# Kernel tuning notes

Hardware: AMD Instinct MI355X
Metric: run time of the kernel (lower is better)

Reference implementation:

```python
import jax, jax.numpy as jnp
import numpy as np
from jax import lax

EMB, HDIM, OBS_LEN = 64, 64, 8
BATCH, NSCENES, SCENE = 32768, 4096, 8
SEQ_LEN = 12


def setup_inputs() -> dict:
    key = jax.random.key(0)
    ks = jax.random.split(key, 16)
    obs_traj = jax.random.normal(ks[0], (OBS_LEN, BATCH, 2), jnp.float32)
    last_pos = jax.random.normal(ks[1], (BATCH, 2), jnp.float32)
    last_pos_rel = jax.random.normal(ks[2], (BATCH, 2), jnp.float32)
    starts = jnp.arange(NSCENES, dtype=jnp.int32) * SCENE
    seq_start_end = jnp.stack([starts, starts + SCENE], axis=1)  # (NSCENES, 2)
    # spatial_embedding: Linear(2, EMB)
    W_se = jax.random.normal(ks[3], (EMB, 2), jnp.float32) * 0.5
    b_se = jax.random.normal(ks[4], (EMB,), jnp.float32) * 0.1
    # weight-normed convs: w = g * v / ||v||_(in,k) per out-channel, bias init zero
    def conv_params(k, cout, cin, ksz):
        ka, kb = jax.random.split(k)
        std = np.sqrt(4.0 / (ksz * cin))
        v = jax.random.normal(ka, (cout, cin, ksz), jnp.float32) * std
        g = jax.random.uniform(kb, (cout,), jnp.float32, 0.5, 1.5)
        b = jnp.zeros((cout,), jnp.float32)
        return v, g, b
    v1, g1, b1 = conv_params(ks[5], HDIM, EMB, 3)
    v2, g2, b2 = conv_params(ks[6], HDIM // 2, HDIM, 3)
    v3, g3, b3 = conv_params(ks[7], HDIM // 2, HDIM // 2, 3)
    # hidden2pos: Linear(2*HDIM, 2)
    W_hp = jax.random.normal(ks[8], (2, 2 * HDIM), jnp.float32) * 0.05
    b_hp = jax.random.normal(ks[9], (2,), jnp.float32) * 0.05
    return {"obs_traj": obs_traj, "last_pos": last_pos, "last_pos_rel": last_pos_rel,
            "W_se": W_se, "b_se": b_se,
            "v1": v1, "g1": g1, "b1": b1,
            "v2": v2, "g2": g2, "b2": b2,
            "v3": v3, "g3": g3, "b3": b3,
            "W_hp": W_hp, "b_hp": b_hp,
            "seq_start_end": seq_start_end, "seq_len": SEQ_LEN}


def _wn_conv_relu(x, v, g, b):
    # weight-norm: w[o] = g[o] * v[o] / ||v[o]||  (norm over in-channels and kernel)
    norm = jnp.sqrt(jnp.sum(v * v, axis=(1, 2)))
    w = v * (g / norm)[:, None, None]
    y = lax.conv_general_dilated(x, w, (1,), 'VALID',
                                 dimension_numbers=('NCH', 'OIH', 'NCH'))
    return jax.nn.relu(y + b[None, :, None])


def reference(obs_traj, last_pos, last_pos_rel,
              W_se, b_se, v1, g1, b1, v2, g2, b2, v3, g3, b3, W_hp, b_hp,
              seq_start_end, seq_len):
    batch = last_pos.shape[0]
    nseg = seq_start_end.shape[0]
    h_dim = v1.shape[0]
    # scene id for each pedestrian (segments are contiguous [start,end) ranges)
    seg = jnp.searchsorted(seq_start_end[:, 0], jnp.arange(batch), side='right') - 1
    # obs_traj embedding -> (batch, EMB, OBS_LEN)
    emb = obs_traj @ W_se.T + b_se            # (T, B, EMB)
    obs_emb0 = jnp.transpose(emb, (1, 2, 0))  # (B, EMB, T)

    def step(carry, _):
        obs_emb, lp = carry
        s = _wn_conv_relu(obs_emb, v1, g1, b1)   # (B, H, T-2)
        s = _wn_conv_relu(s, v2, g2, b2)         # (B, H/2, T-4)
        s = _wn_conv_relu(s, v3, g3, b3)         # (B, H/2, T-6)
        s = s.reshape(batch, h_dim)              # (H/2)*(T-6) == H
        mx = jax.ops.segment_max(s, seg, num_segments=nseg)  # ragged per-scene max
        st = jnp.concatenate([s, mx[seg]], axis=1)           # (B, 2H)
        rel = st @ W_hp.T + b_hp                 # (B, 2)
        lp = rel + lp
        dec = rel @ W_se.T + b_se                # (B, EMB)
        obs_emb = jnp.concatenate([obs_emb[:, :, 1:], dec[:, :, None]], axis=2)
        return (obs_emb, lp), rel

    _, rels = lax.scan(step, (obs_emb0, last_pos), None, length=seq_len)
    return rels  # (seq_len, batch, 2)
```

## Files before the change

kernel.cpp:

```cpp
#include <hip/hip_runtime.h>

#define BATCH 32768
#define SEQLEN 12
#define PEDS 16
#define NBLK (BATCH/PEDS)

typedef short short8 __attribute__((ext_vector_type(8)));
typedef float f32x4 __attribute__((ext_vector_type(4)));

static __device__ __forceinline__ unsigned short f2bf(float x) {
    unsigned u = __float_as_uint(x);
    return (unsigned short)((u + 0x7FFFu + ((u >> 16) & 1u)) >> 16);
}
static __device__ __forceinline__ float bf2f(unsigned short h) {
    return __uint_as_float(((unsigned)h) << 16);
}
static __device__ __forceinline__ int mod6(int h) {
    h = (h >= 12) ? h - 12 : h;
    return (h >= 6) ? h - 6 : h;
}

__global__ __launch_bounds__(256, 3)
void enc_main(const float* __restrict__ obs,
              const float* __restrict__ Wse, const float* __restrict__ bse,
              const float* __restrict__ v1, const float* __restrict__ g1, const float* __restrict__ b1,
              const float* __restrict__ v2, const float* __restrict__ g2, const float* __restrict__ b2,
              const float* __restrict__ v3, const float* __restrict__ g3, const float* __restrict__ b3,
              const float* __restrict__ Whp, const float* __restrict__ bhp,
              float* __restrict__ out)
{
    __shared__ __align__(16) float pos[8][PEDS][2];
    __shared__ __align__(16) unsigned short s1h[6][PEDS][72], s1l[6][PEDS][72];
    __shared__ __align__(16) unsigned short s2h[4][PEDS][40], s2l[4][PEDS][40];
    __shared__ __align__(16) float sff[2][PEDS][68];
    __shared__ __align__(16) float mxs[2][2][68];

    float* wse_s = &sff[0][0][0];
    float* bse_s = wse_s + 128;
    float* sc_s  = wse_s + 192;
    float* a1c   = wse_s + 320;
    float* b1c   = wse_s + 512;
    float* c1c   = wse_s + 704;

    const int tid  = threadIdx.x;
    const int wv   = tid >> 6;
    const int lane = tid & 63;
    const int n    = lane & 15;
    const int kg   = lane >> 4;

    if (tid < 128) wse_s[tid] = Wse[tid];
    else if (tid < 192) bse_s[tid-128] = bse[tid-128];
    if (tid < 64) {
        const float* v = v1 + tid*192; float s = 0.f;
        for (int j = 0; j < 192; j++) s += v[j]*v[j];
        sc_s[tid] = g1[tid] / sqrtf(s);
    } else if (tid < 96) {
        const float* v = v2 + (tid-64)*192; float s = 0.f;
        for (int j = 0; j < 192; j++) s += v[j]*v[j];
        sc_s[tid] = g2[tid-64] / sqrtf(s);
    } else if (tid < 128) {
        const float* v = v3 + (tid-96)*96; float s = 0.f;
        for (int j = 0; j < 96; j++) s += v[j]*v[j];
        sc_s[tid] = g3[tid-96] / sqrtf(s);
    }
    __syncthreads();

    {
        int tau = tid >> 5, p = (tid >> 1) & 15, c = tid & 1;
        pos[tau][p][c] = obs[(tau*BATCH + blockIdx.x*PEDS + p)*2 + c];
    }
    if (tid < 192) {
        int oc = tid & 63, tap = tid >> 6;
        const float* vr = v1 + oc*192 + tap;
        float dA = 0.f, dB = 0.f, dC = 0.f;
        #pragma unroll 8
        for (int ic = 0; ic < 64; ++ic) {
            float w = vr[ic*3];
            dA = fmaf(w, wse_s[ic*2],   dA);
            dB = fmaf(w, wse_s[ic*2+1], dB);
            dC = fmaf(w, bse_s[ic],     dC);
        }
        a1c[tap*64+oc] = dA; b1c[tap*64+oc] = dB; c1c[tap*64+oc] = dC;
    }
    __syncthreads();

    const int c_p = tid >> 4, c_oc0 = (tid & 15) * 4;
    float cA[3][4], cB[3][4], K1[4];
    #pragma unroll
    for (int j = 0; j < 4; ++j) {
        int oc = c_oc0 + j; float s = sc_s[oc];
        float cs = 0.f;
        #pragma unroll
        for (int tap = 0; tap < 3; ++tap) {
            cA[tap][j] = s * a1c[tap*64+oc];
            cB[tap][j] = s * b1c[tap*64+oc];
            cs += c1c[tap*64+oc];
        }
        K1[j] = fmaf(s, cs, b1[oc]);
    }
    short8 wBh[6], wBl[6];
    float  bBr[4];
    if (wv < 2) {
        int oc = wv*16 + n; float s = sc_s[64 + oc];
        #pragma unroll
        for (int kb = 0; kb < 6; ++kb) {
            int tap = kb >> 1, ich = kb & 1;
            #pragma unroll
            for (int j = 0; j < 8; ++j) {
                int ic = ich*32 + kg*8 + j;
                float w = v2[(oc*64 + ic)*3 + tap] * s;
                unsigned short hb = f2bf(w);
                wBh[kb][j] = (short)hb;
                wBl[kb][j] = (short)f2bf(w - bf2f(hb));
            }
        }
        #pragma unroll
        for (int r = 0; r < 4; ++r) bBr[r] = b2[wv*16 + kg*4 + r];
    } else {
        int oc = (wv-2)*16 + n; float s = sc_s[96 + oc];
        #pragma unroll
        for (int kb = 0; kb < 3; ++kb) {
            #pragma unroll
            for (int j = 0; j < 8; ++j) {
                int ic = kg*8 + j;
                float w = v3[(oc*32 + ic)*3 + kb] * s;
                unsigned short hb = f2bf(w);
                wBh[kb][j] = (short)hb;
                wBl[kb][j] = (short)f2bf(w - bf2f(hb));
            }
        }
        #pragma unroll
        for (int r = 0; r < 4; ++r) bBr[r] = b3[(wv-2)*16 + kg*4 + r];
    }
    const int e_p = tid >> 4, e_d = (tid >> 3) & 1, e_sl = tid & 7;
    float wreg[16];
    #pragma unroll
    for (int j = 0; j < 16; ++j) wreg[j] = Whp[e_d*128 + e_sl*16 + j];
    const float bhps = bhp[e_d];

    for (int t = 0; t < 6; ++t) {
        float2 pa = *(const float2*)&pos[t  ][c_p][0];
        float2 pb = *(const float2*)&pos[t+1][c_p][0];
        float2 pc = *(const float2*)&pos[t+2][c_p][0];
        unsigned hw[2], lw[2];
        #pragma unroll
        for (int q = 0; q < 2; ++q) {
            float va, vb;
            {
                int j = q*2;
                va = K1[j];
                va = fmaf(cA[0][j], pa.x, va); va = fmaf(cB[0][j], pa.y, va);
                va = fmaf(cA[1][j], pb.x, va); va = fmaf(cB[1][j], pb.y, va);
                va = fmaf(cA[2][j], pc.x, va); va = fmaf(cB[2][j], pc.y, va);
                va = fmaxf(va, 0.f);
            }
            {
                int j = q*2+1;
                vb = K1[j];
                vb = fmaf(cA[0][j], pa.x, vb); vb = fmaf(cB[0][j], pa.y, vb);
                vb = fmaf(cA[1][j], pb.x, vb); vb = fmaf(cB[1][j], pb.y, vb);
                vb = fmaf(cA[2][j], pc.x, vb); vb = fmaf(cB[2][j], pc.y, vb);
                vb = fmaxf(vb, 0.f);
            }
            unsigned short ha = f2bf(va), hb = f2bf(vb);
            hw[q] = (unsigned)ha | ((unsigned)hb << 16);
            lw[q] = (unsigned)f2bf(va - bf2f(ha)) | ((unsigned)f2bf(vb - bf2f(hb)) << 16);
        }
        *(uint2*)&s1h[t][c_p][c_oc0] = make_uint2(hw[0], hw[1]);
        *(uint2*)&s1l[t][c_p][c_oc0] = make_uint2(lw[0], lw[1]);
    }
    __syncthreads();

    for (int st = 0; st < SEQLEN; ++st) {
        if (wv < 2) {
            for (int t = (st ? 3 : 0); t < 4; ++t) {
                f32x4 a1 = {0.f,0.f,0.f,0.f}, a2 = {0.f,0.f,0.f,0.f}, a3 = {0.f,0.f,0.f,0.f};
                #pragma unroll
                for (int kb = 0; kb < 6; ++kb) {
                    int slot = mod6(st + t + (kb >> 1));
                    int off  = (kb & 1)*32 + kg*8;
                    short8 bh = *(const short8*)&s1h[slot][n][off];
                    short8 bl = *(const short8*)&s1l[slot][n][off];
                    a1 = __builtin_amdgcn_mfma_f32_16x16x32_bf16(wBh[kb], bh, a1, 0, 0, 0);
                    a2 = __builtin_amdgcn_mfma_f32_16x16x32_bf16(wBh[kb], bl, a2, 0, 0, 0);
                    a3 = __builtin_amdgcn_mfma_f32_16x16x32_bf16(wBl[kb], bh, a3, 0, 0, 0);
                }
                int slot2 = (st + t) & 3, oc0 = wv*16 + kg*4;
                float v0 = fmaxf(a1[0]+a2[0]+a3[0]+bBr[0], 0.f);
                float v1_ = fmaxf(a1[1]+a2[1]+a3[1]+bBr[1], 0.f);
                float v2_ = fmaxf(a1[2]+a2[2]+a3[2]+bBr[2], 0.f);
                float v3_ = fmaxf(a1[3]+a2[3]+a3[3]+bBr[3], 0.f);
                unsigned short h0=f2bf(v0), h1=f2bf(v1_), h2=f2bf(v2_), h3=f2bf(v3_);
                *(uint2*)&s2h[slot2][n][oc0] = make_uint2(
                    (unsigned)h0 | ((unsigned)h1 << 16), (unsigned)h2 | ((unsigned)h3 << 16));
                *(uint2*)&s2l[slot2][n][oc0] = make_uint2(
                    (unsigned)f2bf(v0-bf2f(h0)) | ((unsigned)f2bf(v1_-bf2f(h1)) << 16),
                    (unsigned)f2bf(v2_-bf2f(h2)) | ((unsigned)f2bf(v3_-bf2f(h3)) << 16));
            }
        }
        __syncthreads();

        if (wv >= 2) {
            for (int t = (st ? 1 : 0); t < 2; ++t) {
                f32x4 a1 = {0.f,0.f,0.f,0.f}, a2 = {0.f,0.f,0.f,0.f}, a3 = {0.f,0.f,0.f,0.f};
                #pragma unroll
                for (int kb = 0; kb < 3; ++kb) {
                    int slot = (st + t + kb) & 3;
                    short8 bh = *(const short8*)&s2h[slot][n][kg*8];
                    short8 bl = *(const short8*)&s2l[slot][n][kg*8];
                    a1 = __builtin_amdgcn_mfma_f32_16x16x32_bf16(wBh[kb], bh, a1, 0, 0, 0);
                    a2 = __builtin_amdgcn_mfma_f32_16x16x32_bf16(wBh[kb], bl, a2, 0, 0, 0);
                    a3 = __builtin_amdgcn_mfma_f32_16x16x32_bf16(wBl[kb], bh, a3, 0, 0, 0);
                }
                int sl01 = (st + t) & 1, oc0 = (wv-2)*16 + kg*4;
                float m0 = fmaxf(a1[0]+a2[0]+a3[0]+bBr[0], 0.f);
                float m1 = fmaxf(a1[1]+a2[1]+a3[1]+bBr[1], 0.f);
                float m2 = fmaxf(a1[2]+a2[2]+a3[2]+bBr[2], 0.f);
                float m3 = fmaxf(a1[3]+a2[3]+a3[3]+bBr[3], 0.f);
                *(float4*)&sff[sl01][n][oc0] = make_float4(m0, m1, m2, m3);
                #pragma unroll
                for (int msk = 1; msk <= 4; msk <<= 1) {
                    m0 = fmaxf(m0, __shfl_xor(m0, msk));
                    m1 = fmaxf(m1, __shfl_xor(m1, msk));
                    m2 = fmaxf(m2, __shfl_xor(m2, msk));
                    m3 = fmaxf(m3, __shfl_xor(m3, msk));
                }
                if ((n & 7) == 0)
                    *(float4*)&mxs[sl01][n >> 3][oc0] = make_float4(m0, m1, m2, m3);
            }
        }
        __syncthreads();

        {
            int sE = st & 1, sO = (st + 1) & 1;
            float pv;
            if (e_sl < 4) {
                const float* A = &sff[sE][e_p][e_sl*8];
                const float* B = &sff[sO][e_p][e_sl*8];
                float4 a0 = *(const float4*)A, aq = *(const float4*)(A+4);
                float4 b0 = *(const float4*)B, bq = *(const float4*)(B+4);
                pv = wreg[0]*a0.x + wreg[1]*b0.x + wreg[2]*a0.y + wreg[3]*b0.y
                   + wreg[4]*a0.z + wreg[5]*b0.z + wreg[6]*a0.w + wreg[7]*b0.w
                   + wreg[8]*aq.x + wreg[9]*bq.x + wreg[10]*aq.y + wreg[11]*bq.y
                   + wreg[12]*aq.z + wreg[13]*bq.z + wreg[14]*aq.w + wreg[15]*bq.w;
            } else {
                int scn = e_p >> 3;
                const float* A = &mxs[sE][scn][(e_sl-4)*8];
                const float* B = &mxs[sO][scn][(e_sl-4)*8];
                float4 a0 = *(const float4*)A, aq = *(const float4*)(A+4);
                float4 b0 = *(const float4*)B, bq = *(const float4*)(B+4);
                pv = wreg[0]*a0.x + wreg[1]*b0.x + wreg[2]*a0.y + wreg[3]*b0.y
                   + wreg[4]*a0.z + wreg[5]*b0.z + wreg[6]*a0.w + wreg[7]*b0.w
                   + wreg[8]*aq.x + wreg[9]*bq.x + wreg[10]*aq.y + wreg[11]*bq.y
                   + wreg[12]*aq.z + wreg[13]*bq.z + wreg[14]*aq.w + wreg[15]*bq.w;
            }
            pv += __shfl_xor(pv, 1);
            pv += __shfl_xor(pv, 2);
            pv += __shfl_xor(pv, 4);
            float rm = pv + bhps;
            float ro = __shfl_xor(rm, 8);
            float r0 = e_d ? ro : rm;
            float r1 = e_d ? rm : ro;
            if (e_sl == 0)
                out[(st*BATCH + blockIdx.x*PEDS + e_p)*2 + e_d] = rm;
            if (st < SEQLEN-1) {
                float2 pa = *(const float2*)&pos[(st+6)&7][e_p][0];
                float2 pb = *(const float2*)&pos[(st+7)&7][e_p][0];
                int slot5 = mod6(st + 6);
                unsigned hw[2], lw[2];
                #pragma unroll
                for (int q = 0; q < 2; ++q) {
                    float va, vb;
                    {
                        int j = q*2;
                        va = K1[j];
                        va = fmaf(cA[0][j], pa.x, va); va = fmaf(cB[0][j], pa.y, va);
                        va = fmaf(cA[1][j], pb.x, va); va = fmaf(cB[1][j], pb.y, va);
                        va = fmaf(cA[2][j], r0,   va); va = fmaf(cB[2][j], r1,   va);
                        va = fmaxf(va, 0.f);
                    }
                    {
                        int j = q*2+1;
                        vb = K1[j];
                        vb = fmaf(cA[0][j], pa.x, vb); vb = fmaf(cB[0][j], pa.y, vb);
                        vb = fmaf(cA[1][j], pb.x, vb); vb = fmaf(cB[1][j], pb.y, vb);
                        vb = fmaf(cA[2][j], r0,   vb); vb = fmaf(cB[2][j], r1,   vb);
                        vb = fmaxf(vb, 0.f);
                    }
                    unsigned short ha = f2bf(va), hb = f2bf(vb);
                    hw[q] = (unsigned)ha | ((unsigned)hb << 16);
                    lw[q] = (unsigned)f2bf(va - bf2f(ha)) | ((unsigned)f2bf(vb - bf2f(hb)) << 16);
                }
                *(uint2*)&s1h[slot5][c_p][c_oc0] = make_uint2(hw[0], hw[1]);
                *(uint2*)&s1l[slot5][c_p][c_oc0] = make_uint2(lw[0], lw[1]);
                if (e_sl == 0)
                    pos[st & 7][e_p][e_d] = rm;
            }
        }
        __syncthreads();
    }
}

extern "C" void kernel_launch(void* const* d_in, const int* in_sizes, int n_in,
                              void* d_out, int out_size, void* d_ws, size_t ws_size,
                              hipStream_t stream)
{
    const float* obs = (const float*)d_in[0];
    const float* Wse = (const float*)d_in[3];
    const float* bse = (const float*)d_in[4];
    const float* v1  = (const float*)d_in[5];
    const float* g1  = (const float*)d_in[6];
    const float* b1  = (const float*)d_in[7];
    const float* v2  = (const float*)d_in[8];
    const float* g2  = (const float*)d_in[9];
    const float* b2  = (const float*)d_in[10];
    const float* v3  = (const float*)d_in[11];
    const float* g3  = (const float*)d_in[12];
    const float* b3  = (const float*)d_in[13];
    const float* Whp = (const float*)d_in[14];
    const float* bhp = (const float*)d_in[15];

    enc_main<<<NBLK, 256, 0, stream>>>(obs, Wse, bse, v1, g1, b1, v2, g2, b2,
                                       v3, g3, b3, Whp, bhp, (float*)d_out);
}
```

Baseline: 206.7 us.

## Restructure recurrence into two-wave pipeline with MFMA conv1 and register-resident state

The block shrinks from four waves to two. One wave does conv1 (now on MFMA with the weights split into hi and lo bf16 parts) and conv2. The other does conv3, the segment max and the hidden2pos projection, all from registers through shuffles, so the separate output phase and the shared sff/mxs buffers go away. Each step now has two barriers instead of three, ring buffers use &3 instead of mod6, and the bf16 split uses truncation instead of rounding. In exchange each wave carries more serial work and register pressure is higher, and with fewer threads per block there is less parallelism per block.

```diff
diff --git a/kernel.cpp b/kernel.cpp
--- a/kernel.cpp
+++ b/kernel.cpp
@@ -15,12 +15,15 @@
 static __device__ __forceinline__ float bf2f(unsigned short h) {
     return __uint_as_float(((unsigned)h) << 16);
 }
-static __device__ __forceinline__ int mod6(int h) {
-    h = (h >= 12) ? h - 12 : h;
-    return (h >= 6) ? h - 6 : h;
-}
-
-__global__ __launch_bounds__(256, 3)
+static __device__ __forceinline__ void tsplit2(float f0, float f1, unsigned &hw, unsigned &lw) {
+    unsigned u0 = __float_as_uint(f0), u1 = __float_as_uint(f1);
+    float r0 = f0 - __uint_as_float(u0 & 0xFFFF0000u);
+    float r1 = f1 - __uint_as_float(u1 & 0xFFFF0000u);
+    hw = (u0 >> 16) | (u1 & 0xFFFF0000u);
+    lw = (__float_as_uint(r0) >> 16) | (__float_as_uint(r1) & 0xFFFF0000u);
+}
+
+__global__ __launch_bounds__(128)
 void enc_main(const float* __restrict__ obs,
               const float* __restrict__ Wse, const float* __restrict__ bse,
               const float* __restrict__ v1, const float* __restrict__ g1, const float* __restrict__ b1,
@@ -29,27 +32,21 @@
               const float* __restrict__ Whp, const float* __restrict__ bhp,
               float* __restrict__ out)
 {
-    __shared__ __align__(16) float pos[8][PEDS][2];
-    __shared__ __align__(16) unsigned short s1h[6][PEDS][72], s1l[6][PEDS][72];
+    __shared__ __align__(16) unsigned short s1h[4][PEDS][72], s1l[4][PEDS][72];
     __shared__ __align__(16) unsigned short s2h[4][PEDS][40], s2l[4][PEDS][40];
-    __shared__ __align__(16) float sff[2][PEDS][68];
-    __shared__ __align__(16) float mxs[2][2][68];
-
-    float* wse_s = &sff[0][0][0];
-    float* bse_s = wse_s + 128;
-    float* sc_s  = wse_s + 192;
-    float* a1c   = wse_s + 320;
-    float* b1c   = wse_s + 512;
-    float* c1c   = wse_s + 704;
+    __shared__ float relL[PEDS][2];
+    __shared__ float wse_s[128], bse_s[64], sc_s[128];
+    __shared__ float a1c[192], b1c[192], c1c[192];
 
     const int tid  = threadIdx.x;
     const int wv   = tid >> 6;
     const int lane = tid & 63;
     const int n    = lane & 15;
     const int kg   = lane >> 4;
+    const int base = blockIdx.x * PEDS;
 
     if (tid < 128) wse_s[tid] = Wse[tid];
-    else if (tid < 192) bse_s[tid-128] = bse[tid-128];
+    if (tid < 64)  bse_s[tid] = bse[tid];
     if (tid < 64) {
         const float* v = v1 + tid*192; float s = 0.f;
         for (int j = 0; j < 192; j++) s += v[j]*v[j];
@@ -58,19 +55,15 @@
         const float* v = v2 + (tid-64)*192; float s = 0.f;
         for (int j = 0; j < 192; j++) s += v[j]*v[j];
         sc_s[tid] = g2[tid-64] / sqrtf(s);
-    } else if (tid < 128) {
+    } else {
         const float* v = v3 + (tid-96)*96; float s = 0.f;
         for (int j = 0; j < 96; j++) s += v[j]*v[j];
         sc_s[tid] = g3[tid-96] / sqrtf(s);
     }
     __syncthreads();
 
-    {
-        int tau = tid >> 5, p = (tid >> 1) & 15, c = tid & 1;
-        pos[tau][p][c] = obs[(tau*BATCH + blockIdx.x*PEDS + p)*2 + c];
-    }
-    if (tid < 192) {
-        int oc = tid & 63, tap = tid >> 6;
+    for (int idx = tid; idx < 192; idx += 128) {
+        int oc = idx & 63, tap = idx >> 6;
         const float* vr = v1 + oc*192 + tap;
         float dA = 0.f, dB = 0.f, dC = 0.f;
         #pragma unroll 8
@@ -80,222 +73,226 @@
             dB = fmaf(w, wse_s[ic*2+1], dB);
             dC = fmaf(w, bse_s[ic],     dC);
         }
-        a1c[tap*64+oc] = dA; b1c[tap*64+oc] = dB; c1c[tap*64+oc] = dC;
+        a1c[idx] = dA; b1c[idx] = dB; c1c[idx] = dC;
     }
     __syncthreads();
 
-    const int c_p = tid >> 4, c_oc0 = (tid & 15) * 4;
-    float cA[3][4], cB[3][4], K1[4];
-    #pragma unroll
-    for (int j = 0; j < 4; ++j) {
-        int oc = c_oc0 + j; float s = sc_s[oc];
-        float cs = 0.f;
-        #pragma unroll
-        for (int tap = 0; tap < 3; ++tap) {
-            cA[tap][j] = s * a1c[tap*64+oc];
-            cB[tap][j] = s * b1c[tap*64+oc];
-            cs += c1c[tap*64+oc];
-        }
-        K1[j] = fmaf(s, cs, b1[oc]);
+    short8 w2h[2][6], w2l[2][6];  float b2r[2][4];
+    short8 c1f[4];                f32x4 K1r[4];
+    unsigned pa_h=0, pa_l=0, pb_h=0, pb_l=0, pc_h=0, pc_l=0;
+    short8 w3h[2][3], w3l[2][3];  float b3r[2][4];
+    float Wsf[2][2][4][2], Wmx[2][2][4][2];
+    float bhp0=0.f, bhp1=0.f;
+    float prevv[2][4], prevmx[2][4];
+
+    auto conv1_col = [&](int slot, unsigned tAh, unsigned tAl, unsigned tBh, unsigned tBl,
+                         unsigned tCh, unsigned tCl) {
+        union { short8 v; unsigned u[4]; } B;
+        if (kg == 1)      { B.u[0]=tAl; B.u[1]=tBl; B.u[2]=tCl; }
+        else if (kg == 3) { B.u[0]=0u;  B.u[1]=0u;  B.u[2]=0u;  }
+        else              { B.u[0]=tAh; B.u[1]=tBh; B.u[2]=tCh; }
+        B.u[3] = 0u;
+        #pragma unroll
+        for (int T = 0; T < 4; ++T) {
+            f32x4 acc = __builtin_amdgcn_mfma_f32_16x16x32_bf16(c1f[T], B.v, K1r[T], 0, 0, 0);
+            float v0 = fmaxf(acc[0], 0.f), v1_ = fmaxf(acc[1], 0.f);
+            float v2_ = fmaxf(acc[2], 0.f), v3_ = fmaxf(acc[3], 0.f);
+            unsigned hw0, lw0, hw1, lw1;
+            tsplit2(v0, v1_, hw0, lw0);
+            tsplit2(v2_, v3_, hw1, lw1);
+            int o0 = T*16 + kg*4;
+            *(uint2*)&s1h[slot][n][o0] = make_uint2(hw0, hw1);
+            *(uint2*)&s1l[slot][n][o0] = make_uint2(lw0, lw1);
+        }
+    };
+
+    auto conv2_col = [&](int c) {
+        f32x4 A1[2] = {{0,0,0,0},{0,0,0,0}};
+        f32x4 A2[2] = {{0,0,0,0},{0,0,0,0}};
+        f32x4 A3[2] = {{0,0,0,0},{0,0,0,0}};
+        #pragma unroll
+        for (int kb = 0; kb < 6; ++kb) {
+            int slot = (c + (kb >> 1)) & 3;
+            int off  = (kb & 1)*32 + kg*8;
+            short8 bh = *(const short8*)&s1h[slot][n][off];
+            short8 bl = *(const short8*)&s1l[slot][n][off];
+            #pragma unroll
+            for (int T = 0; T < 2; ++T) {
+                A1[T] = __builtin_amdgcn_mfma_f32_16x16x32_bf16(w2h[T][kb], bh, A1[T], 0, 0, 0);
+                A2[T] = __builtin_amdgcn_mfma_f32_16x16x32_bf16(w2h[T][kb], bl, A2[T], 0, 0, 0);
+                A3[T] = __builtin_amdgcn_mfma_f32_16x16x32_bf16(w2l[T][kb], bh, A3[T], 0, 0, 0);
+            }
+        }
+        int s2s = c & 3;
+        #pragma unroll
+        for (int T = 0; T < 2; ++T) {
+            float v0 = fmaxf(A1[T][0]+A2[T][0]+A3[T][0]+b2r[T][0], 0.f);
+            float v1_ = fmaxf(A1[T][1]+A2[T][1]+A3[T][1]+b2r[T][1], 0.f);
+            float v2_ = fmaxf(A1[T][2]+A2[T][2]+A3[T][2]+b2r[T][2], 0.f);
+            float v3_ = fmaxf(A1[T][3]+A2[T][3]+A3[T][3]+b2r[T][3], 0.f);
+            unsigned hw0, lw0, hw1, lw1;
+            tsplit2(v0, v1_, hw0, lw0);
+            tsplit2(v2_, v3_, hw1, lw1);
+            int o0 = T*16 + kg*4;
+            *(uint2*)&s2h[s2s][n][o0] = make_uint2(hw0, hw1);
+            *(uint2*)&s2l[s2s][n][o0] = make_uint2(lw0, lw1);
+        }
+    };
+
+    auto conv3_col = [&](int c, float (&nv)[2][4], float (&nmx)[2][4]) {
+        f32x4 A1[2] = {{0,0,0,0},{0,0,0,0}};
+        f32x4 A2[2] = {{0,0,0,0},{0,0,0,0}};
+        f32x4 A3[2] = {{0,0,0,0},{0,0,0,0}};
+        #pragma unroll
+        for (int kb = 0; kb < 3; ++kb) {
+            int slot = (c + kb) & 3;
+            short8 bh = *(const short8*)&s2h[slot][n][kg*8];
+            short8 bl = *(const short8*)&s2l[slot][n][kg*8];
+            #pragma unroll
+            for (int T = 0; T < 2; ++T) {
+                A1[T] = __builtin_amdgcn_mfma_f32_16x16x32_bf16(w3h[T][kb], bh, A1[T], 0, 0, 0);
+                A2[T] = __builtin_amdgcn_mfma_f32_16x16x32_bf16(w3h[T][kb], bl, A2[T], 0, 0, 0);
+                A3[T] = __builtin_amdgcn_mfma_f32_16x16x32_bf16(w3l[T][kb], bh, A3[T], 0, 0, 0);
+            }
+        }
+        #pragma unroll
+        for (int T = 0; T < 2; ++T)
+            #pragma unroll
+            for (int r = 0; r < 4; ++r) {
+                float m = fmaxf(A1[T][r]+A2[T][r]+A3[T][r]+b3r[T][r], 0.f);
+                nv[T][r] = m;
+                m = fmaxf(m, __shfl_xor(m, 1));
+                m = fmaxf(m, __shfl_xor(m, 2));
+                m = fmaxf(m, __shfl_xor(m, 4));
+                nmx[T][r] = m;
+            }
+    };
+
+    if (wv == 0) {
+        #pragma unroll
+        for (int T = 0; T < 2; ++T) {
+            int oc = T*16 + n; float s = sc_s[64 + oc];
+            #pragma unroll
+            for (int kb = 0; kb < 6; ++kb) {
+                int tap = kb >> 1, ich = kb & 1;
+                #pragma unroll
+                for (int j = 0; j < 8; ++j) {
+                    int ic = ich*32 + kg*8 + j;
+                    float w = v2[(oc*64 + ic)*3 + tap] * s;
+                    unsigned short hb = f2bf(w);
+                    w2h[T][kb][j] = (short)hb;
+                    w2l[T][kb][j] = (short)f2bf(w - bf2f(hb));
+                }
+            }
+            #pragma unroll
+            for (int r = 0; r < 4; ++r) b2r[T][r] = b2[T*16 + kg*4 + r];
+        }
+        #pragma unroll
+        for (int T = 0; T < 4; ++T) {
+            int oc = T*16 + n; float s = sc_s[oc];
+            #pragma unroll
+            for (int j = 0; j < 8; ++j) {
+                float w = 0.f;
+                if (j < 6) {
+                    int tap = j >> 1;
+                    w = s * ((j & 1) ? b1c[tap*64 + oc] : a1c[tap*64 + oc]);
+                }
+                unsigned short hb = f2bf(w);
+                float wl = w - bf2f(hb);
+                c1f[T][j] = (kg <= 1) ? (short)hb : (kg == 2 ? (short)f2bf(wl) : (short)0);
+            }
+            #pragma unroll
+            for (int r = 0; r < 4; ++r) {
+                int o2 = T*16 + kg*4 + r;
+                K1r[T][r] = fmaf(sc_s[o2], c1c[o2] + c1c[64+o2] + c1c[128+o2], b1[o2]);
+            }
+        }
+        unsigned ph[8], pl[8];
+        #pragma unroll
+        for (int tau = 0; tau < 8; ++tau) {
+            float o0 = obs[(tau*BATCH + base + n)*2 + 0];
+            float o1 = obs[(tau*BATCH + base + n)*2 + 1];
+            tsplit2(o0, o1, ph[tau], pl[tau]);
+        }
+        conv1_col(0, ph[0],pl[0], ph[1],pl[1], ph[2],pl[2]);
+        conv1_col(1, ph[1],pl[1], ph[2],pl[2], ph[3],pl[3]);
+        conv1_col(2, ph[2],pl[2], ph[3],pl[3], ph[4],pl[4]);
+        conv1_col(3, ph[3],pl[3], ph[4],pl[4], ph[5],pl[5]);
+        conv2_col(0);
+        conv2_col(1);
+        conv1_col(0, ph[4],pl[4], ph[5],pl[5], ph[6],pl[6]);
+        conv1_col(1, ph[5],pl[5], ph[6],pl[6], ph[7],pl[7]);
+        conv2_col(2);
+        pa_h = ph[5]; pa_l = pl[5]; pb_h = ph[6]; pb_l = pl[6]; pc_h = ph[7]; pc_l = pl[7];
+    } else {
+        #pragma unroll
+        for (int T = 0; T < 2; ++T) {
+            int oc = T*16 + n; float s = sc_s[96 + oc];
+            #pragma unroll
+            for (int kb = 0; kb < 3; ++kb)
+                #pragma unroll
+                for (int j = 0; j < 8; ++j) {
+                    int ic = kg*8 + j;
+                    float w = v3[(oc*32 + ic)*3 + kb] * s;
+                    unsigned short hb = f2bf(w);
+                    w3h[T][kb][j] = (short)hb;
+                    w3l[T][kb][j] = (short)f2bf(w - bf2f(hb));
+                }
+            #pragma unroll
+            for (int r = 0; r < 4; ++r) b3r[T][r] = b3[T*16 + kg*4 + r];
+        }
+        #pragma unroll
+        for (int d2 = 0; d2 < 2; ++d2)
+            #pragma unroll
+            for (int T = 0; T < 2; ++T)
+                #pragma unroll
+                for (int r = 0; r < 4; ++r) {
+                    int oc = T*16 + kg*4 + r;
+                    #pragma unroll
+                    for (int t = 0; t < 2; ++t) {
+                        Wsf[d2][T][r][t] = Whp[d2*128 + oc*2 + t];
+                        Wmx[d2][T][r][t] = Whp[d2*128 + 64 + oc*2 + t];
+                    }
+                }
+        bhp0 = bhp[0]; bhp1 = bhp[1];
     }
-    short8 wBh[6], wBl[6];
-    float  bBr[4];
-    if (wv < 2) {
-        int oc = wv*16 + n; float s = sc_s[64 + oc];
-        #pragma unroll
-        for (int kb = 0; kb < 6; ++kb) {
-            int tap = kb >> 1, ich = kb & 1;
-            #pragma unroll
-            for (int j = 0; j < 8; ++j) {
-                int ic = ich*32 + kg*8 + j;
-                float w = v2[(oc*64 + ic)*3 + tap] * s;
-                unsigned short hb = f2bf(w);
-                wBh[kb][j] = (short)hb;
-                wBl[kb][j] = (short)f2bf(w - bf2f(hb));
-            }
-        }
-        #pragma unroll
-        for (int r = 0; r < 4; ++r) bBr[r] = b2[wv*16 + kg*4 + r];
-    } else {
-        int oc = (wv-2)*16 + n; float s = sc_s[96 + oc];
-        #pragma unroll
-        for (int kb = 0; kb < 3; ++kb) {
-            #pragma unroll
-            for (int j = 0; j < 8; ++j) {
-                int ic = kg*8 + j;
-                float w = v3[(oc*32 + ic)*3 + kb] * s;
-                unsigned short hb = f2bf(w);
-                wBh[kb][j] = (short)hb;
-                wBl[kb][j] = (short)f2bf(w - bf2f(hb));
-            }
-        }
-        #pragma unroll
-        for (int r = 0; r < 4; ++r) bBr[r] = b3[(wv-2)*16 + kg*4 + r];
-    }
-    const int e_p = tid >> 4, e_d = (tid >> 3) & 1, e_sl = tid & 7;
-    float wreg[16];
-    #pragma unroll
-    for (int j = 0; j < 16; ++j) wreg[j] = Whp[e_d*128 + e_sl*16 + j];
-    const float bhps = bhp[e_d];
-
-    for (int t = 0; t < 6; ++t) {
-        float2 pa = *(const float2*)&pos[t  ][c_p][0];
-        float2 pb = *(const float2*)&pos[t+1][c_p][0];
-        float2 pc = *(const float2*)&pos[t+2][c_p][0];
-        unsigned hw[2], lw[2];
-        #pragma unroll
-        for (int q = 0; q < 2; ++q) {
-            float va, vb;
-            {
-                int j = q*2;
-                va = K1[j];
-                va = fmaf(cA[0][j], pa.x, va); va = fmaf(cB[0][j], pa.y, va);
-                va = fmaf(cA[1][j], pb.x, va); va = fmaf(cB[1][j], pb.y, va);
-                va = fmaf(cA[2][j], pc.x, va); va = fmaf(cB[2][j], pc.y, va);
-                va = fmaxf(va, 0.f);
-            }
-            {
-                int j = q*2+1;
-                vb = K1[j];
-                vb = fmaf(cA[0][j], pa.x, vb); vb = fmaf(cB[0][j], pa.y, vb);
-                vb = fmaf(cA[1][j], pb.x, vb); vb = fmaf(cB[1][j], pb.y, vb);
-                vb = fmaf(cA[2][j], pc.x, vb); vb = fmaf(cB[2][j], pc.y, vb);
-                vb = fmaxf(vb, 0.f);
-            }
-            unsigned short ha = f2bf(va), hb = f2bf(vb);
-            hw[q] = (unsigned)ha | ((unsigned)hb << 16);
-            lw[q] = (unsigned)f2bf(va - bf2f(ha)) | ((unsigned)f2bf(vb - bf2f(hb)) << 16);
-        }
-        *(uint2*)&s1h[t][c_p][c_oc0] = make_uint2(hw[0], hw[1]);
-        *(uint2*)&s1l[t][c_p][c_oc0] = make_uint2(lw[0], lw[1]);
-    }
-    __syncthreads();
 
     for (int st = 0; st < SEQLEN; ++st) {
-        if (wv < 2) {
-            for (int t = (st ? 3 : 0); t < 4; ++t) {
-                f32x4 a1 = {0.f,0.f,0.f,0.f}, a2 = {0.f,0.f,0.f,0.f}, a3 = {0.f,0.f,0.f,0.f};
-                #pragma unroll
-                for (int kb = 0; kb < 6; ++kb) {
-                    int slot = mod6(st + t + (kb >> 1));
-                    int off  = (kb & 1)*32 + kg*8;
-                    short8 bh = *(const short8*)&s1h[slot][n][off];
-                    short8 bl = *(const short8*)&s1l[slot][n][off];
-                    a1 = __builtin_amdgcn_mfma_f32_16x16x32_bf16(wBh[kb], bh, a1, 0, 0, 0);
-                    a2 = __builtin_amdgcn_mfma_f32_16x16x32_bf16(wBh[kb], bl, a2, 0, 0, 0);
-                    a3 = __builtin_amdgcn_mfma_f32_16x16x32_bf16(wBl[kb], bh, a3, 0, 0, 0);
-                }
-                int slot2 = (st + t) & 3, oc0 = wv*16 + kg*4;
-                float v0 = fmaxf(a1[0]+a2[0]+a3[0]+bBr[0], 0.f);
-                float v1_ = fmaxf(a1[1]+a2[1]+a3[1]+bBr[1], 0.f);
-                float v2_ = fmaxf(a1[2]+a2[2]+a3[2]+bBr[2], 0.f);
-                float v3_ = fmaxf(a1[3]+a2[3]+a3[3]+bBr[3], 0.f);
-                unsigned short h0=f2bf(v0), h1=f2bf(v1_), h2=f2bf(v2_), h3=f2bf(v3_);
-                *(uint2*)&s2h[slot2][n][oc0] = make_uint2(
-                    (unsigned)h0 | ((unsigned)h1 << 16), (unsigned)h2 | ((unsigned)h3 << 16));
-                *(uint2*)&s2l[slot2][n][oc0] = make_uint2(
-                    (unsigned)f2bf(v0-bf2f(h0)) | ((unsigned)f2bf(v1_-bf2f(h1)) << 16),
-                    (unsigned)f2bf(v2_-bf2f(h2)) | ((unsigned)f2bf(v3_-bf2f(h3)) << 16));
-            }
+        if (wv == 0) {
+            if (st > 0) {
+                float r0 = relL[n][0], r1 = relL[n][1];
+                pa_h = pb_h; pa_l = pb_l; pb_h = pc_h; pb_l = pc_l;
+                tsplit2(r0, r1, pc_h, pc_l);
+                conv1_col((st + 5) & 3, pa_h, pa_l, pb_h, pb_l, pc_h, pc_l);
+            }
+            conv2_col(st + 3);
         }
         __syncthreads();
-
-        if (wv >= 2) {
-            for (int t = (st ? 1 : 0); t < 2; ++t) {
-                f32x4 a1 = {0.f,0.f,0.f,0.f}, a2 = {0.f,0.f,0.f,0.f}, a3 = {0.f,0.f,0.f,0.f};
-                #pragma unroll
-                for (int kb = 0; kb < 3; ++kb) {
-                    int slot = (st + t + kb) & 3;
-                    short8 bh = *(const short8*)&s2h[slot][n][kg*8];
-                    short8 bl = *(const short8*)&s2l[slot][n][kg*8];
-                    a1 = __builtin_amdgcn_mfma_f32_16x16x32_bf16(wBh[kb], bh, a1, 0, 0, 0);
-                    a2 = __builtin_amdgcn_mfma_f32_16x16x32_bf16(wBh[kb], bl, a2, 0, 0, 0);
-                    a3 = __builtin_amdgcn_mfma_f32_16x16x32_bf16(wBl[kb], bh, a3, 0, 0, 0);
-                }
-                int sl01 = (st + t) & 1, oc0 = (wv-2)*16 + kg*4;
-                float m0 = fmaxf(a1[0]+a2[0]+a3[0]+bBr[0], 0.f);
-                float m1 = fmaxf(a1[1]+a2[1]+a3[1]+bBr[1], 0.f);
-                float m2 = fmaxf(a1[2]+a2[2]+a3[2]+bBr[2], 0.f);
-                float m3 = fmaxf(a1[3]+a2[3]+a3[3]+bBr[3], 0.f);
-                *(float4*)&sff[sl01][n][oc0] = make_float4(m0, m1, m2, m3);
-                #pragma unroll
-                for (int msk = 1; msk <= 4; msk <<= 1) {
-                    m0 = fmaxf(m0, __shfl_xor(m0, msk));
-                    m1 = fmaxf(m1, __shfl_xor(m1, msk));
-                    m2 = fmaxf(m2, __shfl_xor(m2, msk));
-                    m3 = fmaxf(m3, __shfl_xor(m3, msk));
-                }
-                if ((n & 7) == 0)
-                    *(float4*)&mxs[sl01][n >> 3][oc0] = make_float4(m0, m1, m2, m3);
-            }
-        }
-        __syncthreads();
-
-        {
-            int sE = st & 1, sO = (st + 1) & 1;
-            float pv;
-            if (e_sl < 4) {
-                const float* A = &sff[sE][e_p][e_sl*8];
-                const float* B = &sff[sO][e_p][e_sl*8];
-                float4 a0 = *(const float4*)A, aq = *(const float4*)(A+4);
-                float4 b0 = *(const float4*)B, bq = *(const float4*)(B+4);
-                pv = wreg[0]*a0.x + wreg[1]*b0.x + wreg[2]*a0.y + wreg[3]*b0.y
-                   + wreg[4]*a0.z + wreg[5]*b0.z + wreg[6]*a0.w + wreg[7]*b0.w
-                   + wreg[8]*aq.x + wreg[9]*bq.x + wreg[10]*aq.y + wreg[11]*bq.y
-                   + wreg[12]*aq.z + wreg[13]*bq.z + wreg[14]*aq.w + wreg[15]*bq.w;
-            } else {
-                int scn = e_p >> 3;
-                const float* A = &mxs[sE][scn][(e_sl-4)*8];
-                const float* B = &mxs[sO][scn][(e_sl-4)*8];
-                float4 a0 = *(const float4*)A, aq = *(const float4*)(A+4);
-                float4 b0 = *(const float4*)B, bq = *(const float4*)(B+4);
-                pv = wreg[0]*a0.x + wreg[1]*b0.x + wreg[2]*a0.y + wreg[3]*b0.y
-                   + wreg[4]*a0.z + wreg[5]*b0.z + wreg[6]*a0.w + wreg[7]*b0.w
-                   + wreg[8]*aq.x + wreg[9]*bq.x + wreg[10]*aq.y + wreg[11]*bq.y
-                   + wreg[12]*aq.z + wreg[13]*bq.z + wreg[14]*aq.w + wreg[15]*bq.w;
-            }
-            pv += __shfl_xor(pv, 1);
-            pv += __shfl_xor(pv, 2);
-            pv += __shfl_xor(pv, 4);
-            float rm = pv + bhps;
-            float ro = __shfl_xor(rm, 8);
-            float r0 = e_d ? ro : rm;
-            float r1 = e_d ? rm : ro;
-            if (e_sl == 0)
-                out[(st*BATCH + blockIdx.x*PEDS + e_p)*2 + e_d] = rm;
-            if (st < SEQLEN-1) {
-                float2 pa = *(const float2*)&pos[(st+6)&7][e_p][0];
-                float2 pb = *(const float2*)&pos[(st+7)&7][e_p][0];
-                int slot5 = mod6(st + 6);
-                unsigned hw[2], lw[2];
-                #pragma unroll
-                for (int q = 0; q < 2; ++q) {
-                    float va, vb;
-                    {
-                        int j = q*2;
-                        va = K1[j];
-                        va = fmaf(cA[0][j], pa.x, va); va = fmaf(cB[0][j], pa.y, va);
-                        va = fmaf(cA[1][j], pb.x, va); va = fmaf(cB[1][j], pb.y, va);
-                        va = fmaf(cA[2][j], r0,   va); va = fmaf(cB[2][j], r1,   va);
-                        va = fmaxf(va, 0.f);
-                    }
-                    {
-                        int j = q*2+1;
-                        vb = K1[j];
-                        vb = fmaf(cA[0][j], pa.x, vb); vb = fmaf(cB[0][j], pa.y, vb);
-                        vb = fmaf(cA[1][j], pb.x, vb); vb = fmaf(cB[1][j], pb.y, vb);
-                        vb = fmaf(cA[2][j], r0,   vb); vb = fmaf(cB[2][j], r1,   vb);
-                        vb = fmaxf(vb, 0.f);
-                    }
-                    unsigned short ha = f2bf(va), hb = f2bf(vb);
-                    hw[q] = (unsigned)ha | ((unsigned)hb << 16);
-                    lw[q] = (unsigned)f2bf(va - bf2f(ha)) | ((unsigned)f2bf(vb - bf2f(hb)) << 16);
-                }
-                *(uint2*)&s1h[slot5][c_p][c_oc0] = make_uint2(hw[0], hw[1]);
-                *(uint2*)&s1l[slot5][c_p][c_oc0] = make_uint2(lw[0], lw[1]);
-                if (e_sl == 0)
-                    pos[st & 7][e_p][e_d] = rm;
-            }
+        if (wv == 1) {
+            float nv[2][4], nmx[2][4];
+            if (st == 0) conv3_col(0, prevv, prevmx);
+            conv3_col(st + 1, nv, nmx);
+            float dd0 = 0.f, dd1 = 0.f;
+            #pragma unroll
+            for (int T = 0; T < 2; ++T)
+                #pragma unroll
+                for (int r = 0; r < 4; ++r) {
+                    dd0 += Wsf[0][T][r][0]*prevv[T][r] + Wsf[0][T][r][1]*nv[T][r]
+                         + Wmx[0][T][r][0]*prevmx[T][r] + Wmx[0][T][r][1]*nmx[T][r];
+                    dd1 += Wsf[1][T][r][0]*prevv[T][r] + Wsf[1][T][r][1]*nv[T][r]
+                         + Wmx[1][T][r][0]*prevmx[T][r] + Wmx[1][T][r][1]*nmx[T][r];
+                }
+            dd0 += __shfl_xor(dd0, 16); dd0 += __shfl_xor(dd0, 32);
+            dd1 += __shfl_xor(dd1, 16); dd1 += __shfl_xor(dd1, 32);
+            float rel0 = dd0 + bhp0, rel1 = dd1 + bhp1;
+            if (kg == 0) {
+                relL[n][0] = rel0; relL[n][1] = rel1;
+                *(float2*)&out[(st*BATCH + base + n)*2] = make_float2(rel0, rel1);
+            }
+            #pragma unroll
+            for (int T = 0; T < 2; ++T)
+                #pragma unroll
+                for (int r = 0; r < 4; ++r) { prevv[T][r] = nv[T][r]; prevmx[T][r] = nmx[T][r]; }
         }
         __syncthreads();
     }
@@ -320,6 +317,6 @@
     const float* Whp = (const float*)d_in[14];
     const float* bhp = (const float*)d_in[15];
 
-    enc_main<<<NBLK, 256, 0, stream>>>(obs, Wse, bse, v1, g1, b1, v2, g2, b2,
+    enc_main<<<NBLK, 128, 0, stream>>>(obs, Wse, bse, v1, g1, b1, v2, g2, b2,
                                        v3, g3, b3, Whp, bhp, (float*)d_out);
 }
```

New measurement: 298.8 us. 44.6% more time.

## Overlap conv3 taps with conv2, shrink conv1 ring, truncate bf16 splits

Applied to the files above, without the earlier changes.

Restructures the per-step schedule. The conv3 warps now issue two of their three taps in the same phase where the conv2 warps compute the new column, and only the final tap runs after the barrier, so the serialized conv3 work shrinks. The conv1 ring buffer shrinks from 6 to 4 slots, which removes the mod6 indexing and cuts LDS use. Launch bounds rise to 4 blocks per CU, and the hi/lo bf16 split now uses truncation instead of round-to-nearest, which is cheaper but slightly changes the rounding of the split values.

```diff
diff --git a/kernel.cpp b/kernel.cpp
--- a/kernel.cpp
+++ b/kernel.cpp
@@ -15,12 +15,15 @@
 static __device__ __forceinline__ float bf2f(unsigned short h) {
     return __uint_as_float(((unsigned)h) << 16);
 }
-static __device__ __forceinline__ int mod6(int h) {
-    h = (h >= 12) ? h - 12 : h;
-    return (h >= 6) ? h - 6 : h;
-}
-
-__global__ __launch_bounds__(256, 3)
+static __device__ __forceinline__ void tsplit2(float f0, float f1, unsigned &hw, unsigned &lw) {
+    unsigned u0 = __float_as_uint(f0), u1 = __float_as_uint(f1);
+    float r0 = f0 - __uint_as_float(u0 & 0xFFFF0000u);
+    float r1 = f1 - __uint_as_float(u1 & 0xFFFF0000u);
+    hw = (u0 >> 16) | (u1 & 0xFFFF0000u);
+    lw = (__float_as_uint(r0) >> 16) | (__float_as_uint(r1) & 0xFFFF0000u);
+}
+
+__global__ __launch_bounds__(256, 4)
 void enc_main(const float* __restrict__ obs,
               const float* __restrict__ Wse, const float* __restrict__ bse,
               const float* __restrict__ v1, const float* __restrict__ g1, const float* __restrict__ b1,
@@ -30,7 +33,7 @@
               float* __restrict__ out)
 {
     __shared__ __align__(16) float pos[8][PEDS][2];
-    __shared__ __align__(16) unsigned short s1h[6][PEDS][72], s1l[6][PEDS][72];
+    __shared__ __align__(16) unsigned short s1h[4][PEDS][72], s1l[4][PEDS][72];
     __shared__ __align__(16) unsigned short s2h[4][PEDS][40], s2l[4][PEDS][40];
     __shared__ __align__(16) float sff[2][PEDS][68];
     __shared__ __align__(16) float mxs[2][2][68];
@@ -138,99 +141,124 @@
     for (int j = 0; j < 16; ++j) wreg[j] = Whp[e_d*128 + e_sl*16 + j];
     const float bhps = bhp[e_d];
 
-    for (int t = 0; t < 6; ++t) {
-        float2 pa = *(const float2*)&pos[t  ][c_p][0];
-        float2 pb = *(const float2*)&pos[t+1][c_p][0];
-        float2 pc = *(const float2*)&pos[t+2][c_p][0];
-        unsigned hw[2], lw[2];
-        #pragma unroll
-        for (int q = 0; q < 2; ++q) {
-            float va, vb;
-            {
-                int j = q*2;
-                va = K1[j];
-                va = fmaf(cA[0][j], pa.x, va); va = fmaf(cB[0][j], pa.y, va);
-                va = fmaf(cA[1][j], pb.x, va); va = fmaf(cB[1][j], pb.y, va);
-                va = fmaf(cA[2][j], pc.x, va); va = fmaf(cB[2][j], pc.y, va);
-                va = fmaxf(va, 0.f);
-            }
-            {
-                int j = q*2+1;
-                vb = K1[j];
-                vb = fmaf(cA[0][j], pa.x, vb); vb = fmaf(cB[0][j], pa.y, vb);
-                vb = fmaf(cA[1][j], pb.x, vb); vb = fmaf(cB[1][j], pb.y, vb);
-                vb = fmaf(cA[2][j], pc.x, vb); vb = fmaf(cB[2][j], pc.y, vb);
-                vb = fmaxf(vb, 0.f);
-            }
-            unsigned short ha = f2bf(va), hb = f2bf(vb);
-            hw[q] = (unsigned)ha | ((unsigned)hb << 16);
-            lw[q] = (unsigned)f2bf(va - bf2f(ha)) | ((unsigned)f2bf(vb - bf2f(hb)) << 16);
-        }
-        *(uint2*)&s1h[t][c_p][c_oc0] = make_uint2(hw[0], hw[1]);
-        *(uint2*)&s1l[t][c_p][c_oc0] = make_uint2(lw[0], lw[1]);
-    }
+    auto conv1_vals = [&](float ax, float ay, float bx, float by,
+                          float cx, float cy, int slot) {
+        float v[4];
+        #pragma unroll
+        for (int j = 0; j < 4; ++j) {
+            float t = K1[j];
+            t = fmaf(cA[0][j], ax, t); t = fmaf(cB[0][j], ay, t);
+            t = fmaf(cA[1][j], bx, t); t = fmaf(cB[1][j], by, t);
+            t = fmaf(cA[2][j], cx, t); t = fmaf(cB[2][j], cy, t);
+            v[j] = fmaxf(t, 0.f);
+        }
+        unsigned hw0, lw0, hw1, lw1;
+        tsplit2(v[0], v[1], hw0, lw0);
+        tsplit2(v[2], v[3], hw1, lw1);
+        *(uint2*)&s1h[slot][c_p][c_oc0] = make_uint2(hw0, hw1);
+        *(uint2*)&s1l[slot][c_p][c_oc0] = make_uint2(lw0, lw1);
+    };
+    auto conv2_col = [&](int c) {
+        f32x4 A1 = {0,0,0,0}, A2 = {0,0,0,0}, A3 = {0,0,0,0};
+        #pragma unroll
+        for (int kb = 0; kb < 6; ++kb) {
+            int slot = (c + (kb >> 1)) & 3;
+            int off  = (kb & 1)*32 + kg*8;
+            short8 bh = *(const short8*)&s1h[slot][n][off];
+            short8 bl = *(const short8*)&s1l[slot][n][off];
+            A1 = __builtin_amdgcn_mfma_f32_16x16x32_bf16(wBh[kb], bh, A1, 0, 0, 0);
+            A2 = __builtin_amdgcn_mfma_f32_16x16x32_bf16(wBh[kb], bl, A2, 0, 0, 0);
+            A3 = __builtin_amdgcn_mfma_f32_16x16x32_bf16(wBl[kb], bh, A3, 0, 0, 0);
+        }
+        int s2s = c & 3, oc0 = wv*16 + kg*4;
+        float v0 = fmaxf(A1[0]+A2[0]+A3[0]+bBr[0], 0.f);
+        float v1_ = fmaxf(A1[1]+A2[1]+A3[1]+bBr[1], 0.f);
+        float v2_ = fmaxf(A1[2]+A2[2]+A3[2]+bBr[2], 0.f);
+        float v3_ = fmaxf(A1[3]+A2[3]+A3[3]+bBr[3], 0.f);
+        unsigned hw0, lw0, hw1, lw1;
+        tsplit2(v0, v1_, hw0, lw0);
+        tsplit2(v2_, v3_, hw1, lw1);
+        *(uint2*)&s2h[s2s][n][oc0] = make_uint2(hw0, hw1);
+        *(uint2*)&s2l[s2s][n][oc0] = make_uint2(lw0, lw1);
+    };
+    auto conv3_tap = [&](int slot, f32x4 &A1, f32x4 &A2, f32x4 &A3, int kb) {
+        short8 bh = *(const short8*)&s2h[slot][n][kg*8];
+        short8 bl = *(const short8*)&s2l[slot][n][kg*8];
+        A1 = __builtin_amdgcn_mfma_f32_16x16x32_bf16(wBh[kb], bh, A1, 0, 0, 0);
+        A2 = __builtin_amdgcn_mfma_f32_16x16x32_bf16(wBh[kb], bl, A2, 0, 0, 0);
+        A3 = __builtin_amdgcn_mfma_f32_16x16x32_bf16(wBl[kb], bh, A3, 0, 0, 0);
+    };
+    auto conv3_epi = [&](f32x4 &A1, f32x4 &A2, f32x4 &A3, int sl01) {
+        int oc0 = (wv-2)*16 + kg*4;
+        float m0 = fmaxf(A1[0]+A2[0]+A3[0]+bBr[0], 0.f);
+        float m1 = fmaxf(A1[1]+A2[1]+A3[1]+bBr[1], 0.f);
+        float m2 = fmaxf(A1[2]+A2[2]+A3[2]+bBr[2], 0.f);
+        float m3 = fmaxf(A1[3]+A2[3]+A3[3]+bBr[3], 0.f);
+        *(float4*)&sff[sl01][n][oc0] = make_float4(m0, m1, m2, m3);
+        #pragma unroll
+        for (int msk = 1; msk <= 4; msk <<= 1) {
+            m0 = fmaxf(m0, __shfl_xor(m0, msk));
+            m1 = fmaxf(m1, __shfl_xor(m1, msk));
+            m2 = fmaxf(m2, __shfl_xor(m2, msk));
+            m3 = fmaxf(m3, __shfl_xor(m3, msk));
+        }
+        if ((n & 7) == 0)
+            *(float4*)&mxs[sl01][n >> 3][oc0] = make_float4(m0, m1, m2, m3);
+    };
+
+    {
+        float2 p0 = *(const float2*)&pos[0][c_p][0];
+        float2 p1 = *(const float2*)&pos[1][c_p][0];
+        float2 p2 = *(const float2*)&pos[2][c_p][0];
+        float2 p3 = *(const float2*)&pos[3][c_p][0];
+        float2 p4 = *(const float2*)&pos[4][c_p][0];
+        float2 p5 = *(const float2*)&pos[5][c_p][0];
+        conv1_vals(p0.x,p0.y, p1.x,p1.y, p2.x,p2.y, 0);
+        conv1_vals(p1.x,p1.y, p2.x,p2.y, p3.x,p3.y, 1);
+        conv1_vals(p2.x,p2.y, p3.x,p3.y, p4.x,p4.y, 2);
+        conv1_vals(p3.x,p3.y, p4.x,p4.y, p5.x,p5.y, 3);
+    }
+    __syncthreads();
+    if (wv < 2) { conv2_col(0); conv2_col(1); }
+    __syncthreads();
+    {
+        float2 p4 = *(const float2*)&pos[4][c_p][0];
+        float2 p5 = *(const float2*)&pos[5][c_p][0];
+        float2 p6 = *(const float2*)&pos[6][c_p][0];
+        float2 p7 = *(const float2*)&pos[7][c_p][0];
+        conv1_vals(p4.x,p4.y, p5.x,p5.y, p6.x,p6.y, 0);
+        conv1_vals(p5.x,p5.y, p6.x,p6.y, p7.x,p7.y, 1);
+    }
+    __syncthreads();
+    if (wv < 2) { conv2_col(2); conv2_col(3); }
     __syncthreads();
 
     for (int st = 0; st < SEQLEN; ++st) {
+        f32x4 C1 = {0,0,0,0}, C2 = {0,0,0,0}, C3 = {0,0,0,0};
         if (wv < 2) {
-            for (int t = (st ? 3 : 0); t < 4; ++t) {
-                f32x4 a1 = {0.f,0.f,0.f,0.f}, a2 = {0.f,0.f,0.f,0.f}, a3 = {0.f,0.f,0.f,0.f};
-                #pragma unroll
-                for (int kb = 0; kb < 6; ++kb) {
-                    int slot = mod6(st + t + (kb >> 1));
-                    int off  = (kb & 1)*32 + kg*8;
-                    short8 bh = *(const short8*)&s1h[slot][n][off];
-                    short8 bl = *(const short8*)&s1l[slot][n][off];
-                    a1 = __builtin_amdgcn_mfma_f32_16x16x32_bf16(wBh[kb], bh, a1, 0, 0, 0);
-                    a2 = __builtin_amdgcn_mfma_f32_16x16x32_bf16(wBh[kb], bl, a2, 0, 0, 0);
-                    a3 = __builtin_amdgcn_mfma_f32_16x16x32_bf16(wBl[kb], bh, a3, 0, 0, 0);
-                }
-                int slot2 = (st + t) & 3, oc0 = wv*16 + kg*4;
-                float v0 = fmaxf(a1[0]+a2[0]+a3[0]+bBr[0], 0.f);
-                float v1_ = fmaxf(a1[1]+a2[1]+a3[1]+bBr[1], 0.f);
-                float v2_ = fmaxf(a1[2]+a2[2]+a3[2]+bBr[2], 0.f);
-                float v3_ = fmaxf(a1[3]+a2[3]+a3[3]+bBr[3], 0.f);
-                unsigned short h0=f2bf(v0), h1=f2bf(v1_), h2=f2bf(v2_), h3=f2bf(v3_);
-                *(uint2*)&s2h[slot2][n][oc0] = make_uint2(
-                    (unsigned)h0 | ((unsigned)h1 << 16), (unsigned)h2 | ((unsigned)h3 << 16));
-                *(uint2*)&s2l[slot2][n][oc0] = make_uint2(
-                    (unsigned)f2bf(v0-bf2f(h0)) | ((unsigned)f2bf(v1_-bf2f(h1)) << 16),
-                    (unsigned)f2bf(v2_-bf2f(h2)) | ((unsigned)f2bf(v3_-bf2f(h3)) << 16));
+            if (st >= 1) conv2_col(st + 3);
+        } else {
+            if (st == 0) {
+                f32x4 B1 = {0,0,0,0}, B2 = {0,0,0,0}, B3 = {0,0,0,0};
+                conv3_tap(0, B1, B2, B3, 0);
+                conv3_tap(1, B1, B2, B3, 1);
+                conv3_tap(2, B1, B2, B3, 2);
+                conv3_epi(B1, B2, B3, 0);
+                conv3_tap(1, C1, C2, C3, 0);
+                conv3_tap(2, C1, C2, C3, 1);
+                conv3_tap(3, C1, C2, C3, 2);
+                conv3_epi(C1, C2, C3, 1);
+            } else {
+                conv3_tap((st + 1) & 3, C1, C2, C3, 0);
+                conv3_tap((st + 2) & 3, C1, C2, C3, 1);
             }
         }
         __syncthreads();
-
-        if (wv >= 2) {
-            for (int t = (st ? 1 : 0); t < 2; ++t) {
-                f32x4 a1 = {0.f,0.f,0.f,0.f}, a2 = {0.f,0.f,0.f,0.f}, a3 = {0.f,0.f,0.f,0.f};
-                #pragma unroll
-                for (int kb = 0; kb < 3; ++kb) {
-                    int slot = (st + t + kb) & 3;
-                    short8 bh = *(const short8*)&s2h[slot][n][kg*8];
-                    short8 bl = *(const short8*)&s2l[slot][n][kg*8];
-                    a1 = __builtin_amdgcn_mfma_f32_16x16x32_bf16(wBh[kb], bh, a1, 0, 0, 0);
-                    a2 = __builtin_amdgcn_mfma_f32_16x16x32_bf16(wBh[kb], bl, a2, 0, 0, 0);
-                    a3 = __builtin_amdgcn_mfma_f32_16x16x32_bf16(wBl[kb], bh, a3, 0, 0, 0);
-                }
-                int sl01 = (st + t) & 1, oc0 = (wv-2)*16 + kg*4;
-                float m0 = fmaxf(a1[0]+a2[0]+a3[0]+bBr[0], 0.f);
-                float m1 = fmaxf(a1[1]+a2[1]+a3[1]+bBr[1], 0.f);
-                float m2 = fmaxf(a1[2]+a2[2]+a3[2]+bBr[2], 0.f);
-                float m3 = fmaxf(a1[3]+a2[3]+a3[3]+bBr[3], 0.f);
-                *(float4*)&sff[sl01][n][oc0] = make_float4(m0, m1, m2, m3);
-                #pragma unroll
-                for (int msk = 1; msk <= 4; msk <<= 1) {
-                    m0 = fmaxf(m0, __shfl_xor(m0, msk));
-                    m1 = fmaxf(m1, __shfl_xor(m1, msk));
-                    m2 = fmaxf(m2, __shfl_xor(m2, msk));
-                    m3 = fmaxf(m3, __shfl_xor(m3, msk));
-                }
-                if ((n & 7) == 0)
-                    *(float4*)&mxs[sl01][n >> 3][oc0] = make_float4(m0, m1, m2, m3);
-            }
+        if (wv >= 2 && st >= 1) {
+            conv3_tap((st + 3) & 3, C1, C2, C3, 2);
+            conv3_epi(C1, C2, C3, (st + 1) & 1);
         }
         __syncthreads();
-
         {
             int sE = st & 1, sO = (st + 1) & 1;
             float pv;
@@ -266,33 +294,7 @@
             if (st < SEQLEN-1) {
                 float2 pa = *(const float2*)&pos[(st+6)&7][e_p][0];
                 float2 pb = *(const float2*)&pos[(st+7)&7][e_p][0];
-                int slot5 = mod6(st + 6);
-                unsigned hw[2], lw[2];
-                #pragma unroll
-                for (int q = 0; q < 2; ++q) {
-                    float va, vb;
-                    {
-                        int j = q*2;
-                        va = K1[j];
-                        va = fmaf(cA[0][j], pa.x, va); va = fmaf(cB[0][j], pa.y, va);
-                        va = fmaf(cA[1][j], pb.x, va); va = fmaf(cB[1][j], pb.y, va);
-                        va = fmaf(cA[2][j], r0,   va); va = fmaf(cB[2][j], r1,   va);
-                        va = fmaxf(va, 0.f);
-                    }
-                    {
-                        int j = q*2+1;
-                        vb = K1[j];
-                        vb = fmaf(cA[0][j], pa.x, vb); vb = fmaf(cB[0][j], pa.y, vb);
-                        vb = fmaf(cA[1][j], pb.x, vb); vb = fmaf(cB[1][j], pb.y, vb);
-                        vb = fmaf(cA[2][j], r0,   vb); vb = fmaf(cB[2][j], r1,   vb);
-                        vb = fmaxf(vb, 0.f);
-                    }
-                    unsigned short ha = f2bf(va), hb = f2bf(vb);
-                    hw[q] = (unsigned)ha | ((unsigned)hb << 16);
-                    lw[q] = (unsigned)f2bf(va - bf2f(ha)) | ((unsigned)f2bf(vb - bf2f(hb)) << 16);
-                }
-                *(uint2*)&s1h[slot5][c_p][c_oc0] = make_uint2(hw[0], hw[1]);
-                *(uint2*)&s1l[slot5][c_p][c_oc0] = make_uint2(lw[0], lw[1]);
+                conv1_vals(pa.x, pa.y, pb.x, pb.y, r0, r1, (st+6)&3);
                 if (e_sl == 0)
                     pos[st & 7][e_p][e_d] = rm;
             }
```

New measurement: 273.8 us. 1.33x slower.
